# Kernel tuning notes

Hardware: AMD Instinct MI355X
Metric: run time of the kernel (lower is better)

The kernel has to match this reference:

```python
import jax, jax.numpy as jnp
import numpy as np

# Architecture search space (matches init_kwargs)
IN_DIMS = (512, 768, 1024)
OUT_MULTS = (2, 3, 4)
MAX_IN = max(IN_DIMS)                       # 1024
MAX_OUT = max(IN_DIMS) * max(OUT_MULTS)     # 4096


def _masks():
    # k iterates (i over IN_DIMS, j over OUT_MULTS) in row-major order, matching
    # the original double loop. Slicing weight[:out_dim, :in_dim] then zero-padding
    # to [MAX_OUT, MAX_IN] is equivalent to multiplying by rank-1 mask
    # row_mask[k] (x) col_mask[k].
    out_dims = np.array([m * i for i in IN_DIMS for m in OUT_MULTS])  # [K=9]
    in_dims = np.array([i for i in IN_DIMS for _ in OUT_MULTS])       # [K=9]
    row_mask = (np.arange(MAX_OUT)[None, :] < out_dims[:, None]).astype(np.float32)  # [K, MAX_OUT]
    col_mask = (np.arange(MAX_IN)[None, :] < in_dims[:, None]).astype(np.float32)    # [K, MAX_IN]
    return jnp.asarray(row_mask), jnp.asarray(col_mask)


def setup_inputs() -> dict:
    key = jax.random.key(0)
    k1, k2, k3, k4 = jax.random.split(key, 4)
    x = jax.random.normal(k1, (8, 4096, MAX_IN), dtype=jnp.float32)
    weights = jax.random.uniform(k2, (9,), dtype=jnp.float32)  # mixing coefficients
    W = jax.random.normal(k3, (MAX_OUT, MAX_IN), dtype=jnp.float32) * 0.02  # linear_layer.weight
    b = jax.random.normal(k4, (MAX_OUT,), dtype=jnp.float32) * 0.02         # linear_layer.bias
    return {"x": x, "weights": weights, "W": W, "b": b}


def reference(x, weights, W, b):
    # weights_mix = sum_k weights[k] * pad(W[:o_k, :i_k]) = W * coeff, where
    # coeff[o, i] = sum_k weights[k] * row_mask[k, o] * col_mask[k, i].
    row_mask, col_mask = _masks()
    coeff = jnp.einsum('k,ko,ki->oi', weights, row_mask, col_mask)  # [MAX_OUT, MAX_IN]
    W_mix = W * coeff
    b_mix = b * (weights @ row_mask)                                # [MAX_OUT]
    # F.linear: y = x @ W_mix.T + b_mix
    return jnp.einsum('bsi,oi->bso', x, W_mix) + b_mix
```

## Files before the change

### kernel.cpp

```cpp
#include <hip/hip_runtime.h>

#define KDIM 1024
#define NDIM 4096

typedef __attribute__((ext_vector_type(4))) float f32x4;
typedef __attribute__((ext_vector_type(8))) short s16x8;
typedef __attribute__((ext_vector_type(8))) unsigned short u16x8;

__device__ __forceinline__ unsigned short f2bf(float f) {
    union { float f; unsigned u; } v; v.f = f;
    unsigned r = v.u + 0x7FFFu + ((v.u >> 16) & 1u);
    return (unsigned short)(r >> 16);
}

#define GLDS(gsrc, ldst)                                                        \
    __builtin_amdgcn_global_load_lds(                                           \
        (const __attribute__((address_space(1))) unsigned int*)(gsrc),          \
        (__attribute__((address_space(3))) unsigned int*)(ldst), 16, 0, 0)

#define SBAR() __builtin_amdgcn_s_barrier()
#define VMW(n) asm volatile("s_waitcnt vmcnt(" #n ")" ::: "memory")
#define LGKM0() asm volatile("s_waitcnt lgkmcnt(0)" ::: "memory")

__device__ __forceinline__ void row_coeffs(int o, const float* w,
                                           float& rp0, float& rp1, float& rp2) {
    rp2 = (o < 2048 ? w[6] : 0.f) + (o < 3072 ? w[7] : 0.f) + w[8];
    rp1 = rp2 + (o < 1536 ? w[3] : 0.f) + (o < 2304 ? w[4] : 0.f) + (o < 3072 ? w[5] : 0.f);
    rp0 = rp1 + (o < 1024 ? w[0] : 0.f) + (o < 1536 ? w[1] : 0.f) + (o < 2048 ? w[2] : 0.f);
}

__device__ __forceinline__ float row_bias_coef(int n, const float* w) {
    return (n < 1024 ? w[0] : 0.f) + (n < 1536 ? w[1] : 0.f)
         + (n < 2048 ? w[2] : 0.f) + (n < 1536 ? w[3] : 0.f)
         + (n < 2304 ? w[4] : 0.f) + (n < 3072 ? w[5] : 0.f)
         + (n < 2048 ? w[6] : 0.f) + (n < 3072 ? w[7] : 0.f) + w[8];
}

__global__ __launch_bounds__(256) void prep_x_p(const float* __restrict__ X,
                                                unsigned short* __restrict__ XB,
                                                int nchunks) {
    const int g = blockIdx.x * 256 + threadIdx.x;
    if (g >= nchunks) return;
    const int c   = g & 1023;
    const int p   = g >> 10;
    const int kt  = p & 31;
    const int mt  = p >> 5;
    const int row = c >> 2;
    const int kcl = (c & 3) ^ ((row >> 1) & 3);
    const float* src = X + ((size_t)(mt * 256 + row) * KDIM + kt * 32 + kcl * 8);
    f32x4 a = *(const f32x4*)src, b = *(const f32x4*)(src + 4);
    u16x8 o;
    o[0] = f2bf(a[0]); o[1] = f2bf(a[1]); o[2] = f2bf(a[2]); o[3] = f2bf(a[3]);
    o[4] = f2bf(b[0]); o[5] = f2bf(b[1]); o[6] = f2bf(b[2]); o[7] = f2bf(b[3]);
    *(u16x8*)(XB + (size_t)g * 8) = o;
}

__global__ __launch_bounds__(256) void prep_w_p(const float* __restrict__ W,
                                                const float* __restrict__ wts,
                                                unsigned short* __restrict__ WB,
                                                int nchunks) {
    const int g = blockIdx.x * 256 + threadIdx.x;
    if (g >= nchunks) return;
    const int c   = g & 1023;
    const int p   = g >> 10;
    const int kt  = p & 31;
    const int nt  = p >> 5;
    const int row = c >> 2;
    const int kcl = (c & 3) ^ ((row >> 1) & 3);
    float w[9];
#pragma unroll
    for (int k = 0; k < 9; ++k) w[k] = wts[k];
    float rp0, rp1, rp2;
    row_coeffs(nt * 256 + row, w, rp0, rp1, rp2);
    const int i0 = kt * 32 + kcl * 8;
    const float cf = i0 < 512 ? rp0 : (i0 < 768 ? rp1 : rp2);
    const float* src = W + ((size_t)(nt * 256 + row) * KDIM + i0);
    f32x4 a = *(const f32x4*)src, b = *(const f32x4*)(src + 4);
    u16x8 o;
    o[0] = f2bf(a[0] * cf); o[1] = f2bf(a[1] * cf); o[2] = f2bf(a[2] * cf); o[3] = f2bf(a[3] * cf);
    o[4] = f2bf(b[0] * cf); o[5] = f2bf(b[1] * cf); o[6] = f2bf(b[2] * cf); o[7] = f2bf(b[3] * cf);
    *(u16x8*)(WB + (size_t)g * 8) = o;
}

__global__ __launch_bounds__(512, 2) void mlv2_gemm_v9(
    const unsigned short* __restrict__ XB,
    const unsigned short* __restrict__ WB,
    const float* __restrict__ wts,
    const float* __restrict__ bias,
    float* __restrict__ Y)
{
    __shared__ unsigned short LDS[4 * 16384];

    const int tid = (int)threadIdx.x;
    const int l   = tid & 63;
    const int w   = tid >> 6;
    const int wm  = w >> 2;
    const int wn  = w & 3;

    const int bid = (int)blockIdx.x;
    const int xcd = bid & 7;
    const int i   = bid >> 3;
    const int n_tile = xcd * 2 + (i & 1);
    const int m_tile = i >> 1;
    const int m0 = m_tile * 256;
    const int n0 = n_tile * 256;

    const int rl = l & 15;
    const unsigned swz = (unsigned)((l >> 4) ^ ((rl >> 1) & 3));
    unsigned offA[8], offB[4];
#pragma unroll
    for (int m = 0; m < 8; ++m)
        offA[m] = ((unsigned)(wm * 128 + m * 16 + rl) * 4u + swz) * 8u;
#pragma unroll
    for (int n = 0; n < 4; ++n)
        offB[n] = 8192u + ((unsigned)(wn * 64 + n * 16 + rl) * 4u + swz) * 8u;

    const unsigned cA0 = (unsigned)(w * 128 + l) * 8u;
    const unsigned cA1 = cA0 + 512u;
    const unsigned dA0 = (unsigned)(w * 1024);
    const unsigned dA1 = dA0 + 512u;
    const unsigned dB0 = 8192u + dA0;
    const unsigned dB1 = 8192u + dA1;

    auto stage = [&](int buf, int kt) {
        const unsigned short* pa = XB + ((size_t)(m_tile * 32 + kt) << 13);
        const unsigned short* pb = WB + ((size_t)(n_tile * 32 + kt) << 13);
        const unsigned ob = (unsigned)buf * 16384u;
        GLDS(pa + cA0, &LDS[ob + dA0]);
        GLDS(pa + cA1, &LDS[ob + dA1]);
        GLDS(pb + cA0, &LDS[ob + dB0]);
        GLDS(pb + cA1, &LDS[ob + dB1]);
    };

    f32x4 acc[8][4];
#pragma unroll
    for (int m = 0; m < 8; ++m)
#pragma unroll
        for (int n = 0; n < 4; ++n) acc[m][n] = (f32x4){0.f, 0.f, 0.f, 0.f};

    auto compute = [&](int buf) {
        const unsigned short* base = &LDS[(unsigned)buf * 16384u];
        s16x8 af[8], bfr[4];
#pragma unroll
        for (int n = 0; n < 4; ++n) bfr[n] = *(const s16x8*)(base + offB[n]);
#pragma unroll
        for (int m = 0; m < 8; ++m) af[m] = *(const s16x8*)(base + offA[m]);
        __builtin_amdgcn_s_setprio(1);
#pragma unroll
        for (int m = 0; m < 8; ++m)
#pragma unroll
            for (int n = 0; n < 4; ++n)
                acc[m][n] = __builtin_amdgcn_mfma_f32_16x16x32_bf16(
                    af[m], bfr[n], acc[m][n], 0, 0, 0);
        __builtin_amdgcn_s_setprio(0);
    };

    stage(0, 0); stage(1, 1); stage(2, 2);
    VMW(8);
    SBAR();

    for (int kt = 0; kt < 29; ++kt) {
        stage((kt + 3) & 3, kt + 3);
        compute(kt & 3);
        VMW(8); LGKM0(); SBAR();
    }
    compute(29 & 3);
    VMW(4); LGKM0(); SBAR();
    compute(30 & 3);
    VMW(0); LGKM0(); SBAR();
    compute(31 & 3);

    float w9[9];
#pragma unroll
    for (int k = 0; k < 9; ++k) w9[k] = wts[k];
    const int gmb = m0 + wm * 128 + (l >> 4) * 4;
    const int gnb = n0 + wn * 64 + rl;
#pragma unroll
    for (int n = 0; n < 4; ++n) {
        const int gn = gnb + n * 16;
        const float bc = bias[gn] * row_bias_coef(gn, w9);
#pragma unroll
        for (int m = 0; m < 8; ++m) {
            float* yp = Y + (size_t)(gmb + m * 16) * NDIM + gn;
            yp[0 * NDIM] = acc[m][n][0] + bc;
            yp[1 * NDIM] = acc[m][n][1] + bc;
            yp[2 * NDIM] = acc[m][n][2] + bc;
            yp[3 * NDIM] = acc[m][n][3] + bc;
        }
    }
}

__global__ __launch_bounds__(256, 2) void mlv2_gemm_v1(
    const float* __restrict__ X, const float* __restrict__ wts,
    const float* __restrict__ W, const float* __restrict__ bias,
    float* __restrict__ Y)
{
    __shared__ unsigned short Alds[2][4][128][8];
    __shared__ unsigned short Blds[2][4][128][8];
    const int tid = (int)threadIdx.x;
    const int bid = (int)blockIdx.x;
    const int wg  = (bid & 7) * 1024 + (bid >> 3);
    const int n_tile = wg & 31;
    const int m_tile = wg >> 5;
    float w[9];
#pragma unroll
    for (int k = 0; k < 9; ++k) w[k] = wts[k];
    const int srow = tid >> 1;
    const int scol = (tid & 1) << 4;
    const int kc0  = (tid & 1) << 1;
    const float* xp = X + (size_t)(m_tile * 128 + srow) * KDIM + scol;
    const float* wp = W + (size_t)(n_tile * 128 + srow) * KDIM + scol;
    const int orow = n_tile * 128 + srow;
    float rp0, rp1, rp2;
    row_coeffs(orow, w, rp0, rp1, rp2);
    const int lane = tid & 63, wv = tid >> 6;
    const int frow = lane & 15, kcl = lane >> 4;
    const int arow0 = (wv >> 1) * 64 + frow;
    const int brow0 = (wv & 1) * 64 + frow;
    auto coef = [&](int t) -> float { return t < 16 ? rp0 : (t < 24 ? rp1 : rp2); };
    auto stage_load = [&](int t, f32x4 a[4], f32x4 b[4]) {
        const f32x4* xq = (const f32x4*)(xp + t * 32);
        const f32x4* wq = (const f32x4*)(wp + t * 32);
#pragma unroll
        for (int j = 0; j < 4; ++j) { a[j] = xq[j]; b[j] = wq[j]; }
    };
    auto stage_write = [&](int buf, const f32x4 a[4], const f32x4 b[4], float cf) {
        u16x8 va[2], vb[2];
#pragma unroll
        for (int j = 0; j < 4; ++j)
#pragma unroll
            for (int e = 0; e < 4; ++e) {
                const int idx = j * 4 + e;
                va[idx >> 3][idx & 7] = f2bf(a[j][e]);
                vb[idx >> 3][idx & 7] = f2bf(b[j][e] * cf);
            }
        *(u16x8*)&Alds[buf][kc0    ][srow][0] = va[0];
        *(u16x8*)&Alds[buf][kc0 + 1][srow][0] = va[1];
        *(u16x8*)&Blds[buf][kc0    ][srow][0] = vb[0];
        *(u16x8*)&Blds[buf][kc0 + 1][srow][0] = vb[1];
    };
    f32x4 acc[4][4];
#pragma unroll
    for (int i = 0; i < 4; ++i)
#pragma unroll
        for (int j = 0; j < 4; ++j) acc[i][j] = (f32x4){0.f, 0.f, 0.f, 0.f};
    {
        f32x4 a[4], b[4];
        stage_load(0, a, b);
        stage_write(0, a, b, coef(0));
    }
    __syncthreads();
    const int NT = KDIM / 32;
    int cur = 0;
    for (int t = 0; t < NT; ++t) {
        f32x4 a[4], b[4];
        if (t + 1 < NT) stage_load(t + 1, a, b);
        s16x8 af[4], bf_[4];
#pragma unroll
        for (int i = 0; i < 4; ++i) {
            af[i]  = *(const s16x8*)&Alds[cur][kcl][arow0 + i * 16][0];
            bf_[i] = *(const s16x8*)&Blds[cur][kcl][brow0 + i * 16][0];
        }
#pragma unroll
        for (int i = 0; i < 4; ++i)
#pragma unroll
            for (int j = 0; j < 4; ++j)
                acc[i][j] = __builtin_amdgcn_mfma_f32_16x16x32_bf16(
                    af[i], bf_[j], acc[i][j], 0, 0, 0);
        if (t + 1 < NT) stage_write(cur ^ 1, a, b, coef(t + 1));
        __syncthreads();
        cur ^= 1;
    }
    const int gm0 = m_tile * 128 + (wv >> 1) * 64 + kcl * 4;
    const int gn0 = n_tile * 128 + (wv & 1) * 64 + frow;
#pragma unroll
    for (int j = 0; j < 4; ++j) {
        const int n = gn0 + j * 16;
        const float bc = bias[n] * row_bias_coef(n, w);
#pragma unroll
        for (int i = 0; i < 4; ++i) {
            float* yp = Y + (size_t)(gm0 + i * 16) * NDIM + n;
            yp[0 * NDIM] = acc[i][j][0] + bc;
            yp[1 * NDIM] = acc[i][j][1] + bc;
            yp[2 * NDIM] = acc[i][j][2] + bc;
            yp[3 * NDIM] = acc[i][j][3] + bc;
        }
    }
}

extern "C" void kernel_launch(void* const* d_in, const int* in_sizes, int n_in,
                              void* d_out, int out_size, void* d_ws, size_t ws_size,
                              hipStream_t stream) {
    const float* X    = (const float*)d_in[0];
    const float* wts  = (const float*)d_in[1];
    const float* W    = (const float*)d_in[2];
    const float* bias = (const float*)d_in[3];
    float* Y = (float*)d_out;

    const int M = in_sizes[0] / KDIM;

    const size_t xb_elems = (size_t)M * KDIM;
    const size_t wb_elems = (size_t)NDIM * KDIM;
    const size_t ws_needed = (xb_elems + wb_elems) * sizeof(unsigned short);

    if (ws_size >= ws_needed && (M % 256) == 0) {
        unsigned short* XB = (unsigned short*)d_ws;
        unsigned short* WB = XB + xb_elems;
        const int xchunks = (int)(xb_elems / 8);
        const int wchunks = (int)(wb_elems / 8);
        prep_x_p<<<(xchunks + 255) / 256, 256, 0, stream>>>(X, XB, xchunks);
        prep_w_p<<<(wchunks + 255) / 256, 256, 0, stream>>>(W, wts, WB, wchunks);
        const int grid = (M / 256) * (NDIM / 256);
        mlv2_gemm_v9<<<grid, 512, 0, stream>>>(XB, WB, wts, bias, Y);
    } else {
        const int grid = (M / 128) * (NDIM / 128);
        mlv2_gemm_v1<<<grid, 256, 0, stream>>>(X, wts, W, bias, Y);
    }
}
```

Measured before the change: 377.6 us.

## Shrink GEMM M-tile to 128 with triple-buffered LDS for higher occupancy

Changes the bf16 GEMM block tile from 256x256 to 128x256, so each wave holds a 4x4 accumulator set instead of 8x4. LDS pipelining drops from four buffers to three rotating buffers, and launch bounds now target four blocks per CU. The X pre-pack kernel is relaid out for 128-row tiles to match. The aim is more resident waves and a larger grid to hide latency, at the cost of lower arithmetic intensity per block and more W-tile reloads from memory.

```diff
diff --git a/kernel.cpp b/kernel.cpp
--- a/kernel.cpp
+++ b/kernel.cpp
@@ -41,13 +41,13 @@
                                                 int nchunks) {
     const int g = blockIdx.x * 256 + threadIdx.x;
     if (g >= nchunks) return;
-    const int c   = g & 1023;
-    const int p   = g >> 10;
+    const int c   = g & 511;
+    const int p   = g >> 9;
     const int kt  = p & 31;
     const int mt  = p >> 5;
     const int row = c >> 2;
     const int kcl = (c & 3) ^ ((row >> 1) & 3);
-    const float* src = X + ((size_t)(mt * 256 + row) * KDIM + kt * 32 + kcl * 8);
+    const float* src = X + ((size_t)(mt * 128 + row) * KDIM + kt * 32 + kcl * 8);
     f32x4 a = *(const f32x4*)src, b = *(const f32x4*)(src + 4);
     u16x8 o;
     o[0] = f2bf(a[0]); o[1] = f2bf(a[1]); o[2] = f2bf(a[2]); o[3] = f2bf(a[3]);
@@ -82,14 +82,14 @@
     *(u16x8*)(WB + (size_t)g * 8) = o;
 }
 
-__global__ __launch_bounds__(512, 2) void mlv2_gemm_v9(
+__global__ __launch_bounds__(512, 4) void mlv2_gemm_v10(
     const unsigned short* __restrict__ XB,
     const unsigned short* __restrict__ WB,
     const float* __restrict__ wts,
     const float* __restrict__ bias,
     float* __restrict__ Y)
 {
-    __shared__ unsigned short LDS[4 * 16384];
+    __shared__ unsigned short LDS[3 * 12288];
 
     const int tid = (int)threadIdx.x;
     const int l   = tid & 63;
@@ -102,85 +102,83 @@
     const int i   = bid >> 3;
     const int n_tile = xcd * 2 + (i & 1);
     const int m_tile = i >> 1;
-    const int m0 = m_tile * 256;
+    const int m0 = m_tile * 128;
     const int n0 = n_tile * 256;
 
     const int rl = l & 15;
     const unsigned swz = (unsigned)((l >> 4) ^ ((rl >> 1) & 3));
-    unsigned offA[8], offB[4];
-#pragma unroll
-    for (int m = 0; m < 8; ++m)
-        offA[m] = ((unsigned)(wm * 128 + m * 16 + rl) * 4u + swz) * 8u;
+    unsigned offA[4], offB[4];
+#pragma unroll
+    for (int m = 0; m < 4; ++m)
+        offA[m] = ((unsigned)(wm * 64 + m * 16 + rl) * 4u + swz) * 8u;
 #pragma unroll
     for (int n = 0; n < 4; ++n)
-        offB[n] = 8192u + ((unsigned)(wn * 64 + n * 16 + rl) * 4u + swz) * 8u;
-
-    const unsigned cA0 = (unsigned)(w * 128 + l) * 8u;
-    const unsigned cA1 = cA0 + 512u;
-    const unsigned dA0 = (unsigned)(w * 1024);
-    const unsigned dA1 = dA0 + 512u;
-    const unsigned dB0 = 8192u + dA0;
-    const unsigned dB1 = 8192u + dA1;
-
-    auto stage = [&](int buf, int kt) {
-        const unsigned short* pa = XB + ((size_t)(m_tile * 32 + kt) << 13);
+        offB[n] = 4096u + ((unsigned)(wn * 64 + n * 16 + rl) * 4u + swz) * 8u;
+
+    const unsigned cA  = (unsigned)(w * 64 + l) * 8u;
+    const unsigned cB0 = (unsigned)(w * 128 + l) * 8u;
+    const unsigned cB1 = cB0 + 512u;
+    const unsigned dA  = (unsigned)(w * 512);
+    const unsigned dB0 = 4096u + (unsigned)(w * 1024);
+    const unsigned dB1 = dB0 + 512u;
+
+    auto stage = [&](unsigned ob, int kt) {
+        const unsigned short* pa = XB + ((size_t)(m_tile * 32 + kt) << 12);
         const unsigned short* pb = WB + ((size_t)(n_tile * 32 + kt) << 13);
-        const unsigned ob = (unsigned)buf * 16384u;
-        GLDS(pa + cA0, &LDS[ob + dA0]);
-        GLDS(pa + cA1, &LDS[ob + dA1]);
-        GLDS(pb + cA0, &LDS[ob + dB0]);
-        GLDS(pb + cA1, &LDS[ob + dB1]);
+        GLDS(pa + cA,  &LDS[ob + dA]);
+        GLDS(pb + cB0, &LDS[ob + dB0]);
+        GLDS(pb + cB1, &LDS[ob + dB1]);
     };
 
-    f32x4 acc[8][4];
-#pragma unroll
-    for (int m = 0; m < 8; ++m)
+    f32x4 acc[4][4];
+#pragma unroll
+    for (int m = 0; m < 4; ++m)
 #pragma unroll
         for (int n = 0; n < 4; ++n) acc[m][n] = (f32x4){0.f, 0.f, 0.f, 0.f};
 
-    auto compute = [&](int buf) {
-        const unsigned short* base = &LDS[(unsigned)buf * 16384u];
-        s16x8 af[8], bfr[4];
-#pragma unroll
-        for (int n = 0; n < 4; ++n) bfr[n] = *(const s16x8*)(base + offB[n]);
-#pragma unroll
-        for (int m = 0; m < 8; ++m) af[m] = *(const s16x8*)(base + offA[m]);
+    auto compute = [&](unsigned ob) {
+        const unsigned short* base = &LDS[ob];
+        s16x8 a[4], b[4];
+#pragma unroll
+        for (int n = 0; n < 4; ++n) b[n] = *(const s16x8*)(base + offB[n]);
+#pragma unroll
+        for (int m = 0; m < 4; ++m) a[m] = *(const s16x8*)(base + offA[m]);
         __builtin_amdgcn_s_setprio(1);
 #pragma unroll
-        for (int m = 0; m < 8; ++m)
+        for (int m = 0; m < 4; ++m)
 #pragma unroll
             for (int n = 0; n < 4; ++n)
                 acc[m][n] = __builtin_amdgcn_mfma_f32_16x16x32_bf16(
-                    af[m], bfr[n], acc[m][n], 0, 0, 0);
+                    a[m], b[n], acc[m][n], 0, 0, 0);
         __builtin_amdgcn_s_setprio(0);
     };
 
-    stage(0, 0); stage(1, 1); stage(2, 2);
-    VMW(8);
+    unsigned o0 = 0, o1 = 12288, o2 = 24576;
+    stage(o0, 0); stage(o1, 1);
+    VMW(3);
     SBAR();
 
-    for (int kt = 0; kt < 29; ++kt) {
-        stage((kt + 3) & 3, kt + 3);
-        compute(kt & 3);
-        VMW(8); LGKM0(); SBAR();
-    }
-    compute(29 & 3);
-    VMW(4); LGKM0(); SBAR();
-    compute(30 & 3);
+    for (int kt = 0; kt < 30; ++kt) {
+        stage(o2, kt + 2);
+        compute(o0);
+        VMW(3); LGKM0(); SBAR();
+        const unsigned t_ = o0; o0 = o1; o1 = o2; o2 = t_;
+    }
+    compute(o0);
     VMW(0); LGKM0(); SBAR();
-    compute(31 & 3);
+    compute(o1);
 
     float w9[9];
 #pragma unroll
     for (int k = 0; k < 9; ++k) w9[k] = wts[k];
-    const int gmb = m0 + wm * 128 + (l >> 4) * 4;
+    const int gmb = m0 + wm * 64 + (l >> 4) * 4;
     const int gnb = n0 + wn * 64 + rl;
 #pragma unroll
     for (int n = 0; n < 4; ++n) {
         const int gn = gnb + n * 16;
         const float bc = bias[gn] * row_bias_coef(gn, w9);
 #pragma unroll
-        for (int m = 0; m < 8; ++m) {
+        for (int m = 0; m < 4; ++m) {
             float* yp = Y + (size_t)(gmb + m * 16) * NDIM + gn;
             yp[0 * NDIM] = acc[m][n][0] + bc;
             yp[1 * NDIM] = acc[m][n][1] + bc;
@@ -303,15 +301,15 @@
     const size_t wb_elems = (size_t)NDIM * KDIM;
     const size_t ws_needed = (xb_elems + wb_elems) * sizeof(unsigned short);
 
-    if (ws_size >= ws_needed && (M % 256) == 0) {
+    if (ws_size >= ws_needed && (M % 128) == 0) {
         unsigned short* XB = (unsigned short*)d_ws;
         unsigned short* WB = XB + xb_elems;
         const int xchunks = (int)(xb_elems / 8);
         const int wchunks = (int)(wb_elems / 8);
         prep_x_p<<<(xchunks + 255) / 256, 256, 0, stream>>>(X, XB, xchunks);
         prep_w_p<<<(wchunks + 255) / 256, 256, 0, stream>>>(W, wts, WB, wchunks);
-        const int grid = (M / 256) * (NDIM / 256);
-        mlv2_gemm_v9<<<grid, 512, 0, stream>>>(XB, WB, wts, bias, Y);
+        const int grid = (M / 128) * (NDIM / 256);
+        mlv2_gemm_v10<<<grid, 512, 0, stream>>>(XB, WB, wts, bias, Y);
     } else {
         const int grid = (M / 128) * (NDIM / 128);
         mlv2_gemm_v1<<<grid, 256, 0, stream>>>(X, wts, W, bias, Y);
```

Measured after the change: 369.1 us. 1.02x faster.

## Switch GEMM to 32x32x16 MFMA with register double-buffered LDS reads

Applied to the files above, without the earlier changes.

The main GEMM kernel now uses 32x32x16 bf16 MFMA tiles instead of 16x16x32. It prefetches the next k-tile's fragments into a second register set while the current one computes, which removes the per-iteration lgkmcnt(0) wait. The prep kernels store data k-chunk-major (row = c&255) without the XOR swizzle, to match the new LDS read pattern. Fewer, larger MFMAs and overlapped LDS reads should improve matrix-core utilisation. In exchange, register pressure rises, the unswizzled layout may cause LDS bank conflicts, and output stores are now strided by row.

```diff
diff --git a/kernel.cpp b/kernel.cpp
--- a/kernel.cpp
+++ b/kernel.cpp
@@ -4,6 +4,7 @@
 #define NDIM 4096
 
 typedef __attribute__((ext_vector_type(4))) float f32x4;
+typedef __attribute__((ext_vector_type(16))) float f32x16;
 typedef __attribute__((ext_vector_type(8))) short s16x8;
 typedef __attribute__((ext_vector_type(8))) unsigned short u16x8;
 
@@ -20,7 +21,6 @@
 
 #define SBAR() __builtin_amdgcn_s_barrier()
 #define VMW(n) asm volatile("s_waitcnt vmcnt(" #n ")" ::: "memory")
-#define LGKM0() asm volatile("s_waitcnt lgkmcnt(0)" ::: "memory")
 
 __device__ __forceinline__ void row_coeffs(int o, const float* w,
                                            float& rp0, float& rp1, float& rp2) {
@@ -45,9 +45,9 @@
     const int p   = g >> 10;
     const int kt  = p & 31;
     const int mt  = p >> 5;
-    const int row = c >> 2;
-    const int kcl = (c & 3) ^ ((row >> 1) & 3);
-    const float* src = X + ((size_t)(mt * 256 + row) * KDIM + kt * 32 + kcl * 8);
+    const int row = c & 255;
+    const int kc  = c >> 8;
+    const float* src = X + ((size_t)(mt * 256 + row) * KDIM + kt * 32 + kc * 8);
     f32x4 a = *(const f32x4*)src, b = *(const f32x4*)(src + 4);
     u16x8 o;
     o[0] = f2bf(a[0]); o[1] = f2bf(a[1]); o[2] = f2bf(a[2]); o[3] = f2bf(a[3]);
@@ -65,14 +65,14 @@
     const int p   = g >> 10;
     const int kt  = p & 31;
     const int nt  = p >> 5;
-    const int row = c >> 2;
-    const int kcl = (c & 3) ^ ((row >> 1) & 3);
+    const int row = c & 255;
+    const int kc  = c >> 8;
     float w[9];
 #pragma unroll
     for (int k = 0; k < 9; ++k) w[k] = wts[k];
     float rp0, rp1, rp2;
     row_coeffs(nt * 256 + row, w, rp0, rp1, rp2);
-    const int i0 = kt * 32 + kcl * 8;
+    const int i0 = kt * 32 + kc * 8;
     const float cf = i0 < 512 ? rp0 : (i0 < 768 ? rp1 : rp2);
     const float* src = W + ((size_t)(nt * 256 + row) * KDIM + i0);
     f32x4 a = *(const f32x4*)src, b = *(const f32x4*)(src + 4);
@@ -82,7 +82,7 @@
     *(u16x8*)(WB + (size_t)g * 8) = o;
 }
 
-__global__ __launch_bounds__(512, 2) void mlv2_gemm_v9(
+__global__ __launch_bounds__(512, 2) void mlv2_gemm_v11(
     const unsigned short* __restrict__ XB,
     const unsigned short* __restrict__ WB,
     const float* __restrict__ wts,
@@ -105,87 +105,107 @@
     const int m0 = m_tile * 256;
     const int n0 = n_tile * 256;
 
-    const int rl = l & 15;
-    const unsigned swz = (unsigned)((l >> 4) ^ ((rl >> 1) & 3));
-    unsigned offA[8], offB[4];
-#pragma unroll
-    for (int m = 0; m < 8; ++m)
-        offA[m] = ((unsigned)(wm * 128 + m * 16 + rl) * 4u + swz) * 8u;
-#pragma unroll
-    for (int n = 0; n < 4; ++n)
-        offB[n] = 8192u + ((unsigned)(wn * 64 + n * 16 + rl) * 4u + swz) * 8u;
-
-    const unsigned cA0 = (unsigned)(w * 128 + l) * 8u;
-    const unsigned cA1 = cA0 + 512u;
+    const unsigned kg    = (unsigned)(l >> 5);
+    const unsigned baseA = kg * 2048u + (unsigned)(wm * 128 + (l & 31)) * 8u;
+    const unsigned baseB = 8192u + kg * 2048u + (unsigned)(wn * 64 + (l & 31)) * 8u;
+
+    const unsigned cS  = (unsigned)(w * 128 + l) * 8u;
     const unsigned dA0 = (unsigned)(w * 1024);
     const unsigned dA1 = dA0 + 512u;
     const unsigned dB0 = 8192u + dA0;
-    const unsigned dB1 = 8192u + dA1;
-
-    auto stage = [&](int buf, int kt) {
+    const unsigned dB1 = dB0 + 512u;
+
+    auto stage = [&](int kt) {
         const unsigned short* pa = XB + ((size_t)(m_tile * 32 + kt) << 13);
         const unsigned short* pb = WB + ((size_t)(n_tile * 32 + kt) << 13);
-        const unsigned ob = (unsigned)buf * 16384u;
-        GLDS(pa + cA0, &LDS[ob + dA0]);
-        GLDS(pa + cA1, &LDS[ob + dA1]);
-        GLDS(pb + cA0, &LDS[ob + dB0]);
-        GLDS(pb + cA1, &LDS[ob + dB1]);
-    };
-
-    f32x4 acc[8][4];
-#pragma unroll
-    for (int m = 0; m < 8; ++m)
-#pragma unroll
-        for (int n = 0; n < 4; ++n) acc[m][n] = (f32x4){0.f, 0.f, 0.f, 0.f};
-
-    auto compute = [&](int buf) {
-        const unsigned short* base = &LDS[(unsigned)buf * 16384u];
-        s16x8 af[8], bfr[4];
-#pragma unroll
-        for (int n = 0; n < 4; ++n) bfr[n] = *(const s16x8*)(base + offB[n]);
-#pragma unroll
-        for (int m = 0; m < 8; ++m) af[m] = *(const s16x8*)(base + offA[m]);
+        const unsigned ob = (unsigned)(kt & 3) * 16384u;
+        GLDS(pa + cS,        &LDS[ob + dA0]);
+        GLDS(pa + cS + 512u, &LDS[ob + dA1]);
+        GLDS(pb + cS,        &LDS[ob + dB0]);
+        GLDS(pb + cS + 512u, &LDS[ob + dB1]);
+    };
+
+    f32x16 acc[4][2];
+#pragma unroll
+    for (int mt = 0; mt < 4; ++mt)
+#pragma unroll
+        for (int nt = 0; nt < 2; ++nt)
+#pragma unroll
+            for (int r = 0; r < 16; ++r) acc[mt][nt][r] = 0.f;
+
+    s16x8 aX[4][2], bX[2][2], aY[4][2], bY[2][2];
+
+    auto rd = [&](s16x8 (&a)[4][2], s16x8 (&b)[2][2], int kt) {
+        const unsigned ob = (unsigned)(kt & 3) * 16384u;
+        const unsigned short* pA = &LDS[ob + baseA];
+        const unsigned short* pB = &LDS[ob + baseB];
+#pragma unroll
+        for (int ks = 0; ks < 2; ++ks) {
+#pragma unroll
+            for (int mt = 0; mt < 4; ++mt)
+                a[mt][ks] = *(const s16x8*)(pA + ks * 4096 + mt * 256);
+#pragma unroll
+            for (int nt = 0; nt < 2; ++nt)
+                b[nt][ks] = *(const s16x8*)(pB + ks * 4096 + nt * 256);
+        }
+    };
+    auto mm = [&](const s16x8 (&a)[4][2], const s16x8 (&b)[2][2]) {
         __builtin_amdgcn_s_setprio(1);
 #pragma unroll
-        for (int m = 0; m < 8; ++m)
-#pragma unroll
-            for (int n = 0; n < 4; ++n)
-                acc[m][n] = __builtin_amdgcn_mfma_f32_16x16x32_bf16(
-                    af[m], bfr[n], acc[m][n], 0, 0, 0);
+        for (int ks = 0; ks < 2; ++ks)
+#pragma unroll
+            for (int mt = 0; mt < 4; ++mt)
+#pragma unroll
+                for (int nt = 0; nt < 2; ++nt)
+                    acc[mt][nt] = __builtin_amdgcn_mfma_f32_32x32x16_bf16(
+                        a[mt][ks], b[nt][ks], acc[mt][nt], 0, 0, 0);
         __builtin_amdgcn_s_setprio(0);
     };
 
-    stage(0, 0); stage(1, 1); stage(2, 2);
-    VMW(8);
+    stage(0); stage(1); stage(2);
+    VMW(4);
     SBAR();
-
-    for (int kt = 0; kt < 29; ++kt) {
-        stage((kt + 3) & 3, kt + 3);
-        compute(kt & 3);
-        VMW(8); LGKM0(); SBAR();
-    }
-    compute(29 & 3);
-    VMW(4); LGKM0(); SBAR();
-    compute(30 & 3);
-    VMW(0); LGKM0(); SBAR();
-    compute(31 & 3);
+    rd(aX, bX, 0);
+
+    for (int kt = 0; kt < 28; kt += 2) {
+        stage(kt + 3);
+        rd(aY, bY, kt + 1);
+        mm(aX, bX);
+        VMW(4); SBAR();
+
+        stage(kt + 4);
+        rd(aX, bX, kt + 2);
+        mm(aY, bY);
+        VMW(4); SBAR();
+    }
+    stage(31);
+    rd(aY, bY, 29);
+    mm(aX, bX);
+    VMW(4); SBAR();
+    rd(aX, bX, 30);
+    mm(aY, bY);
+    VMW(0); SBAR();
+    rd(aY, bY, 31);
+    mm(aX, bX);
+    mm(aY, bY);
 
     float w9[9];
 #pragma unroll
     for (int k = 0; k < 9; ++k) w9[k] = wts[k];
-    const int gmb = m0 + wm * 128 + (l >> 4) * 4;
-    const int gnb = n0 + wn * 64 + rl;
-#pragma unroll
-    for (int n = 0; n < 4; ++n) {
-        const int gn = gnb + n * 16;
+    const int colb = l & 31;
+    const int rhi  = (l >> 5) * 4;
+#pragma unroll
+    for (int nt = 0; nt < 2; ++nt) {
+        const int gn = n0 + wn * 64 + nt * 32 + colb;
         const float bc = bias[gn] * row_bias_coef(gn, w9);
 #pragma unroll
-        for (int m = 0; m < 8; ++m) {
-            float* yp = Y + (size_t)(gmb + m * 16) * NDIM + gn;
-            yp[0 * NDIM] = acc[m][n][0] + bc;
-            yp[1 * NDIM] = acc[m][n][1] + bc;
-            yp[2 * NDIM] = acc[m][n][2] + bc;
-            yp[3 * NDIM] = acc[m][n][3] + bc;
+        for (int mt = 0; mt < 4; ++mt) {
+            const int rb = m0 + wm * 128 + mt * 32 + rhi;
+#pragma unroll
+            for (int r = 0; r < 16; ++r) {
+                const int row = rb + (r & 3) + 8 * (r >> 2);
+                Y[(size_t)row * NDIM + gn] = acc[mt][nt][r] + bc;
+            }
         }
     }
 }
@@ -311,7 +331,7 @@
         prep_x_p<<<(xchunks + 255) / 256, 256, 0, stream>>>(X, XB, xchunks);
         prep_w_p<<<(wchunks + 255) / 256, 256, 0, stream>>>(W, wts, WB, wchunks);
         const int grid = (M / 256) * (NDIM / 256);
-        mlv2_gemm_v9<<<grid, 512, 0, stream>>>(XB, WB, wts, bias, Y);
+        mlv2_gemm_v11<<<grid, 512, 0, stream>>>(XB, WB, wts, bias, Y);
     } else {
         const int grid = (M / 128) * (NDIM / 128);
         mlv2_gemm_v1<<<grid, 256, 0, stream>>>(X, wts, W, bias, Y);
```

New measurement: 412.4 us. 1.09x slower.

## Split GEMM main loop into two ping-pong phases interleaving loads and MFMAs

Applied to the files above, without the earlier changes.

Restructures the bf16 GEMM main loop so each K-tile runs as two phases. Each phase issues half of the global-to-LDS staging (A or B), reads a subset of fragments and runs 16 MFMAs, with barriers and sched_barrier fences between phases. The aim is to interleave LDS reads, global loads and matrix work across waves, in a ping-pong style, instead of one large load-then-compute block per iteration. The cost is extra barriers per K step and tighter sync ordering, which could add stalls.

```diff
diff --git a/kernel.cpp b/kernel.cpp
--- a/kernel.cpp
+++ b/kernel.cpp
@@ -20,7 +20,8 @@
 
 #define SBAR() __builtin_amdgcn_s_barrier()
 #define VMW(n) asm volatile("s_waitcnt vmcnt(" #n ")" ::: "memory")
-#define LGKM0() asm volatile("s_waitcnt lgkmcnt(0)" ::: "memory")
+#define LG0()  do { asm volatile("s_waitcnt lgkmcnt(0)" ::: "memory");          \
+                    __builtin_amdgcn_sched_barrier(0); } while (0)
 
 __device__ __forceinline__ void row_coeffs(int o, const float* w,
                                            float& rp0, float& rp1, float& rp2) {
@@ -82,7 +83,7 @@
     *(u16x8*)(WB + (size_t)g * 8) = o;
 }
 
-__global__ __launch_bounds__(512, 2) void mlv2_gemm_v9(
+__global__ __launch_bounds__(512, 2) void mlv2_gemm_v12(
     const unsigned short* __restrict__ XB,
     const unsigned short* __restrict__ WB,
     const float* __restrict__ wts,
@@ -115,21 +116,23 @@
     for (int n = 0; n < 4; ++n)
         offB[n] = 8192u + ((unsigned)(wn * 64 + n * 16 + rl) * 4u + swz) * 8u;
 
-    const unsigned cA0 = (unsigned)(w * 128 + l) * 8u;
-    const unsigned cA1 = cA0 + 512u;
+    const unsigned cS  = (unsigned)(w * 128 + l) * 8u;
     const unsigned dA0 = (unsigned)(w * 1024);
     const unsigned dA1 = dA0 + 512u;
     const unsigned dB0 = 8192u + dA0;
-    const unsigned dB1 = 8192u + dA1;
-
-    auto stage = [&](int buf, int kt) {
+    const unsigned dB1 = dB0 + 512u;
+
+    auto stageA = [&](int kt) {
         const unsigned short* pa = XB + ((size_t)(m_tile * 32 + kt) << 13);
+        const unsigned ob = (unsigned)(kt & 3) * 16384u;
+        GLDS(pa + cS,        &LDS[ob + dA0]);
+        GLDS(pa + cS + 512u, &LDS[ob + dA1]);
+    };
+    auto stageB = [&](int kt) {
         const unsigned short* pb = WB + ((size_t)(n_tile * 32 + kt) << 13);
-        const unsigned ob = (unsigned)buf * 16384u;
-        GLDS(pa + cA0, &LDS[ob + dA0]);
-        GLDS(pa + cA1, &LDS[ob + dA1]);
-        GLDS(pb + cA0, &LDS[ob + dB0]);
-        GLDS(pb + cA1, &LDS[ob + dB1]);
+        const unsigned ob = (unsigned)(kt & 3) * 16384u;
+        GLDS(pb + cS,        &LDS[ob + dB0]);
+        GLDS(pb + cS + 512u, &LDS[ob + dB1]);
     };
 
     f32x4 acc[8][4];
@@ -138,37 +141,56 @@
 #pragma unroll
         for (int n = 0; n < 4; ++n) acc[m][n] = (f32x4){0.f, 0.f, 0.f, 0.f};
 
-    auto compute = [&](int buf) {
-        const unsigned short* base = &LDS[(unsigned)buf * 16384u];
-        s16x8 af[8], bfr[4];
-#pragma unroll
-        for (int n = 0; n < 4; ++n) bfr[n] = *(const s16x8*)(base + offB[n]);
-#pragma unroll
-        for (int m = 0; m < 8; ++m) af[m] = *(const s16x8*)(base + offA[m]);
+    s16x8 bf4[4], af4[4];
+
+    auto phA = [&](int kt, bool st) {
+        const unsigned short* base = &LDS[(unsigned)(kt & 3) * 16384u];
+        if (st) stageA(kt + 3);
+#pragma unroll
+        for (int n = 0; n < 4; ++n) bf4[n] = *(const s16x8*)(base + offB[n]);
+#pragma unroll
+        for (int m = 0; m < 4; ++m) af4[m] = *(const s16x8*)(base + offA[m]);
+        SBAR();
+        LG0();
         __builtin_amdgcn_s_setprio(1);
 #pragma unroll
-        for (int m = 0; m < 8; ++m)
+        for (int m = 0; m < 4; ++m)
 #pragma unroll
             for (int n = 0; n < 4; ++n)
                 acc[m][n] = __builtin_amdgcn_mfma_f32_16x16x32_bf16(
-                    af[m], bfr[n], acc[m][n], 0, 0, 0);
+                    af4[m], bf4[n], acc[m][n], 0, 0, 0);
         __builtin_amdgcn_s_setprio(0);
-    };
-
-    stage(0, 0); stage(1, 1); stage(2, 2);
-    VMW(8);
+        SBAR();
+    };
+    auto phB = [&](int kt, bool st) {
+        const unsigned short* base = &LDS[(unsigned)(kt & 3) * 16384u];
+        if (st) stageB(kt + 3);
+#pragma unroll
+        for (int m = 0; m < 4; ++m) af4[m] = *(const s16x8*)(base + offA[m + 4]);
+        SBAR();
+        LG0();
+        __builtin_amdgcn_s_setprio(1);
+#pragma unroll
+        for (int m = 0; m < 4; ++m)
+#pragma unroll
+            for (int n = 0; n < 4; ++n)
+                acc[m + 4][n] = __builtin_amdgcn_mfma_f32_16x16x32_bf16(
+                    af4[m], bf4[n], acc[m + 4][n], 0, 0, 0);
+        __builtin_amdgcn_s_setprio(0);
+    };
+
+    stageA(0); stageB(0); stageA(1); stageB(1); stageA(2); stageB(2);
+    VMW(6);
     SBAR();
 
     for (int kt = 0; kt < 29; ++kt) {
-        stage((kt + 3) & 3, kt + 3);
-        compute(kt & 3);
-        VMW(8); LGKM0(); SBAR();
-    }
-    compute(29 & 3);
-    VMW(4); LGKM0(); SBAR();
-    compute(30 & 3);
-    VMW(0); LGKM0(); SBAR();
-    compute(31 & 3);
+        phA(kt, true);
+        phB(kt, true);
+        VMW(6); SBAR();
+    }
+    phA(29, false); phB(29, false); VMW(4); SBAR();
+    phA(30, false); phB(30, false); VMW(0); SBAR();
+    phA(31, false); phB(31, false);
 
     float w9[9];
 #pragma unroll
@@ -311,7 +333,7 @@
         prep_x_p<<<(xchunks + 255) / 256, 256, 0, stream>>>(X, XB, xchunks);
         prep_w_p<<<(wchunks + 255) / 256, 256, 0, stream>>>(W, wts, WB, wchunks);
         const int grid = (M / 256) * (NDIM / 256);
-        mlv2_gemm_v9<<<grid, 512, 0, stream>>>(XB, WB, wts, bias, Y);
+        mlv2_gemm_v12<<<grid, 512, 0, stream>>>(XB, WB, wts, bias, Y);
     } else {
         const int grid = (M / 128) * (NDIM / 128);
         mlv2_gemm_v1<<<grid, 256, 0, stream>>>(X, wts, W, bias, Y);
```

Result: no change. 381.7 us (+1.1%).
